# Kernel tuning notes

Hardware: AMD Instinct MI355X
Metric: run time of the kernel (lower is better)

The kernel has to match this reference:

```python
import jax, jax.numpy as jnp
import numpy as np
from math import factorial as _f

LMAX = 2
META = [128, 128, 128]  # input channels per l


def _cg_complex(l1, l2, l3):
    """Condon-Shortley complex Clebsch-Gordan coefficients <l3 m3 | l1 m1 l2 m2>."""
    C = np.zeros((2 * l1 + 1, 2 * l2 + 1, 2 * l3 + 1))
    for m1 in range(-l1, l1 + 1):
        for m2 in range(-l2, l2 + 1):
            m3 = m1 + m2
            if abs(m3) > l3:
                continue
            pre = ((2 * l3 + 1) * _f(l1 + l2 - l3) * _f(l1 - l2 + l3) * _f(-l1 + l2 + l3) / _f(l1 + l2 + l3 + 1)) ** 0.5
            pre *= (_f(l3 + m3) * _f(l3 - m3) * _f(l1 - m1) * _f(l1 + m1) * _f(l2 - m2) * _f(l2 + m2)) ** 0.5
            s = 0.0
            for k in range(0, l1 + l2 - l3 + 1):
                den = [k, l1 + l2 - l3 - k, l1 - m1 - k, l2 + m2 - k, l3 - l2 + m1 + k, l3 - l1 - m2 + k]
                if min(den) < 0:
                    continue
                d = 1.0
                for t in den:
                    d *= _f(t)
                s += (-1) ** k / d
            C[m1 + l1, m2 + l2, m3 + l3] = pre * s
    return C


def _u(l):
    """Complex -> real spherical harmonic change of basis, rows = real m index."""
    U = np.zeros((2 * l + 1, 2 * l + 1), dtype=np.complex128)
    U[l, l] = 1.0
    for m in range(1, l + 1):
        U[l + m, l + m] = (-1) ** m / np.sqrt(2.0)
        U[l + m, l - m] = 1.0 / np.sqrt(2.0)
        U[l - m, l - m] = 1j / np.sqrt(2.0)
        U[l - m, l + m] = -1j * (-1) ** m / np.sqrt(2.0)
    return U


def _cg_real(l1, l2, l3):
    C = _cg_complex(l1, l2, l3).astype(np.complex128)
    R = np.einsum('ai,bj,ck,ijk->abc', _u(l1), _u(l2), np.conj(_u(l3)), C)
    # real-basis CG is purely real or purely imaginary depending on parity of l1+l2+l3
    R = R.imag if np.abs(R.imag).max() > np.abs(R.real).max() else R.real
    return R.astype(np.float32)


# valid couplings (lout-major order, matching the cat layout consumed by repids_tp_out)
LOUT_MAX = 2 * LMAX
COUPLINGS = []
for _lo in range(LOUT_MAX + 1):
    for _l1 in range(LMAX + 1):
        for _l2 in range(LMAX + 1):
            if abs(_l1 - _l2) <= _lo <= _l1 + _l2 and META[_l1] > 0 and META[_l2] > 0:
                COUPLINGS.append((_lo, _l1, _l2, min(META[_l1], META[_l2])))
MIX_OFFS = np.cumsum([0] + [c[3] for c in COUPLINGS])[:-1]
NUM_MIX = int(sum(c[3] for c in COUPLINGS))  # 2432
META_OUT = [max([d for (lo, _, _, d) in COUPLINGS if lo == l], default=0) for l in range(LOUT_MAX + 1)]
CGT = {(l1, l2, lo): _cg_real(l1, l2, lo) for (lo, l1, l2, _) in COUPLINGS}
DIM_IN = int(sum((2 * l + 1) * META[l] for l in range(LMAX + 1)))   # 1152
DIM_OUT = int(sum((2 * l + 1) * META_OUT[l] for l in range(LOUT_MAX + 1)))  # 3200
SQ3 = 3.0 ** 0.5


def setup_inputs() -> dict:
    key = jax.random.key(0)
    k1, k2, k3 = jax.random.split(key, 3)
    B = 16384
    x = jax.random.normal(k1, (B, DIM_IN), dtype=jnp.float32)
    keep_coeff = jax.random.uniform(k2, (sum(META),), dtype=jnp.float32, minval=-SQ3, maxval=SQ3)
    mix_coeff = jax.random.uniform(k3, (NUM_MIX,), dtype=jnp.float32, minval=-SQ3, maxval=SQ3)
    return {"x": x, "keep_coeff": keep_coeff, "mix_coeff": mix_coeff}


def reference(x, keep_coeff, mix_coeff):
    B = x.shape[0]
    # split input rep into per-l blocks, layout is m-major / channel-minor: (B, 2l+1, n_l)
    xs, keep_xs = [], []
    off, coff = 0, 0
    for l in range(LMAX + 1):
        n = META[l]
        sz = (2 * l + 1) * n
        xl = x[:, off:off + sz].reshape(B, 2 * l + 1, n)
        xs.append(xl)
        keep_xs.append(xl * keep_coeff[coff:coff + n])  # k_l \odot x^(l)
        off += sz
        coff += n
    out_blocks = [jnp.zeros((B, 2 * l + 1, META_OUT[l]), x.dtype) for l in range(LOUT_MAX + 1)]
    # CG tensor-product path: 0.5 * s \odot (x ⊗ x), overlapping couplings to same lout are summed
    for (lout, l1, l2, deg), moff in zip(COUPLINGS, MIX_OFFS):
        cg = jnp.asarray(CGT[(l1, l2, lout)])  # (2l1+1, 2l2+1, 2lout+1)
        tp = jnp.einsum('bic,bjc,ijk->bkc', xs[l1][:, :, :deg], xs[l2][:, :, :deg], cg)
        tp = tp * (0.5 * mix_coeff[int(moff):int(moff) + deg])
        out_blocks[lout] = out_blocks[lout].at[:, :, :deg].add(tp)
    # keep (skip) path: copy scaled input channels into the output layout
    for l in range(LMAX + 1):
        ncp = min(META[l], META_OUT[l])
        out_blocks[l] = out_blocks[l].at[:, :, :ncp].add(keep_xs[l][:, :, :ncp])
    return jnp.concatenate([b.reshape(B, -1) for b in out_blocks], axis=1)
```

## Files before the change

### kernel.cpp

```cpp
#include <hip/hip_runtime.h>

namespace cgx {

struct Cplx { double re, im; };

constexpr Cplx cmul(Cplx a, Cplx b) {
  return Cplx{a.re * b.re - a.im * b.im, a.re * b.im + a.im * b.re};
}

constexpr double cfact(int n) {
  double r = 1.0;
  for (int i = 2; i <= n; i++) r *= (double)i;
  return r;
}

constexpr double cabs_(double x) { return x < 0.0 ? -x : x; }

constexpr double csqrt_(double x) {
  if (x <= 0.0) return 0.0;
  double g = x > 1.0 ? x : 1.0;
  for (int it = 0; it < 80; ++it) g = 0.5 * (g + x / g);
  return g;
}

struct CGC { double v[5][5][9]; };

constexpr CGC cg_complex(int l1, int l2, int l3) {
  CGC C{};
  for (int m1 = -l1; m1 <= l1; m1++) {
    for (int m2 = -l2; m2 <= l2; m2++) {
      int m3 = m1 + m2;
      if (m3 < -l3 || m3 > l3) continue;
      double pre = csqrt_((double)(2 * l3 + 1) * cfact(l1 + l2 - l3) *
                          cfact(l1 - l2 + l3) * cfact(-l1 + l2 + l3) /
                          cfact(l1 + l2 + l3 + 1));
      pre *= csqrt_(cfact(l3 + m3) * cfact(l3 - m3) * cfact(l1 - m1) *
                    cfact(l1 + m1) * cfact(l2 - m2) * cfact(l2 + m2));
      double s = 0.0;
      for (int k = 0; k <= l1 + l2 - l3; k++) {
        int d1 = l1 + l2 - l3 - k, d2 = l1 - m1 - k, d3 = l2 + m2 - k;
        int d4 = l3 - l2 + m1 + k, d5 = l3 - l1 - m2 + k;
        if (d1 < 0 || d2 < 0 || d3 < 0 || d4 < 0 || d5 < 0) continue;
        double d = cfact(k) * cfact(d1) * cfact(d2) * cfact(d3) * cfact(d4) * cfact(d5);
        s += ((k & 1) ? -1.0 : 1.0) / d;
      }
      C.v[m1 + l1][m2 + l2][m3 + l3] = pre * s;
    }
  }
  return C;
}

struct UMat { Cplx v[9][9]; };

constexpr UMat umat(int l) {
  UMat U{};
  double is2 = csqrt_(0.5);
  U.v[l][l] = Cplx{1.0, 0.0};
  for (int m = 1; m <= l; m++) {
    double sgn = (m & 1) ? -1.0 : 1.0;
    U.v[l + m][l + m] = Cplx{sgn * is2, 0.0};
    U.v[l + m][l - m] = Cplx{is2, 0.0};
    U.v[l - m][l - m] = Cplx{0.0, is2};
    U.v[l - m][l + m] = Cplx{0.0, -sgn * is2};
  }
  return U;
}

struct CGR { float v[5][5][9]; };

constexpr CGR cg_real(int l1, int l2, int l3) {
  CGC C = cg_complex(l1, l2, l3);
  UMat U1 = umat(l1), U2 = umat(l2), U3 = umat(l3);
  double re[5][5][9]{}, im[5][5][9]{};
  double maxre = 0.0, maxim = 0.0;
  for (int a = 0; a < 2 * l1 + 1; a++)
    for (int b = 0; b < 2 * l2 + 1; b++)
      for (int c = 0; c < 2 * l3 + 1; c++) {
        double ar = 0.0, ai = 0.0;
        for (int i = 0; i < 2 * l1 + 1; i++) {
          Cplx u1 = U1.v[a][i];
          if (u1.re == 0.0 && u1.im == 0.0) continue;
          for (int j = 0; j < 2 * l2 + 1; j++) {
            Cplx u2 = U2.v[b][j];
            if (u2.re == 0.0 && u2.im == 0.0) continue;
            int k0 = (i - l1) + (j - l2) + l3;
            if (k0 < 0 || k0 > 2 * l3) continue;
            double cv = C.v[i][j][k0];
            if (cv == 0.0) continue;
            Cplx u3 = U3.v[c][k0];
            if (u3.re == 0.0 && u3.im == 0.0) continue;
            Cplx u12 = cmul(u1, u2);
            Cplx t = cmul(u12, Cplx{u3.re, -u3.im});
            ar += t.re * cv;
            ai += t.im * cv;
          }
        }
        re[a][b][c] = ar;
        im[a][b][c] = ai;
        if (cabs_(ar) > maxre) maxre = cabs_(ar);
        if (cabs_(ai) > maxim) maxim = cabs_(ai);
      }
  CGR R{};
  bool useim = maxim > maxre;
  for (int a = 0; a < 2 * l1 + 1; a++)
    for (int b = 0; b < 2 * l2 + 1; b++)
      for (int c = 0; c < 2 * l3 + 1; c++)
        R.v[a][b][c] = (float)(useim ? im[a][b][c] : re[a][b][c]);
  return R;
}

}

template <int L1, int L2, int LO>
__device__ __forceinline__ void do_coupling(const float* xa, const float* xb,
                                            float halfmix, float* out) {
  constexpr cgx::CGR t = cgx::cg_real(L1, L2, LO);
#pragma unroll
  for (int k = 0; k < 2 * LO + 1; k++) {
    float tp = 0.0f;
#pragma unroll
    for (int i = 0; i < 2 * L1 + 1; i++) {
#pragma unroll
      for (int j = 0; j < 2 * L2 + 1; j++) {
        const float cv = t.v[i][j][k];
        if (cv > 1e-7f || cv < -1e-7f)
          tp = fmaf(cv * xa[i], xb[j], tp);
      }
    }
    out[k] = fmaf(halfmix, tp, out[k]);
  }
}


__global__ __launch_bounds__(256) void selfmix_kernel(
    const float* __restrict__ x, const float* __restrict__ keep,
    const float* __restrict__ mix, float* __restrict__ out, int B) {
  int tid = blockIdx.x * 256 + threadIdx.x;
  int b = tid >> 7;
  int c = tid & 127;
  if (b >= B) return;

  const float* xb = x + (size_t)b * 1152;
  float x0a[1];
  float x1[3], x2[5];
  x0a[0] = xb[c];
#pragma unroll
  for (int m = 0; m < 3; m++) x1[m] = xb[128 + m * 128 + c];
#pragma unroll
  for (int m = 0; m < 5; m++) x2[m] = xb[512 + m * 128 + c];

  float mx[19];
#pragma unroll
  for (int i = 0; i < 19; i++) mx[i] = 0.5f * mix[i * 128 + c];

  float o0[1], o1[3], o2[5], o3[7], o4[9];
  o0[0] = keep[c] * x0a[0];
  float k1 = keep[128 + c];
#pragma unroll
  for (int m = 0; m < 3; m++) o1[m] = k1 * x1[m];
  float k2 = keep[256 + c];
#pragma unroll
  for (int m = 0; m < 5; m++) o2[m] = k2 * x2[m];
#pragma unroll
  for (int m = 0; m < 7; m++) o3[m] = 0.0f;
#pragma unroll
  for (int m = 0; m < 9; m++) o4[m] = 0.0f;

  do_coupling<0, 0, 0>(x0a, x0a, mx[0], o0);
  do_coupling<1, 1, 0>(x1, x1, mx[1], o0);
  do_coupling<2, 2, 0>(x2, x2, mx[2], o0);

  do_coupling<0, 1, 1>(x0a, x1, mx[3], o1);
  do_coupling<1, 0, 1>(x1, x0a, mx[4], o1);
  do_coupling<1, 1, 1>(x1, x1, mx[5], o1);
  do_coupling<1, 2, 1>(x1, x2, mx[6], o1);
  do_coupling<2, 1, 1>(x2, x1, mx[7], o1);
  do_coupling<2, 2, 1>(x2, x2, mx[8], o1);

  do_coupling<0, 2, 2>(x0a, x2, mx[9], o2);
  do_coupling<1, 1, 2>(x1, x1, mx[10], o2);
  do_coupling<1, 2, 2>(x1, x2, mx[11], o2);
  do_coupling<2, 0, 2>(x2, x0a, mx[12], o2);
  do_coupling<2, 1, 2>(x2, x1, mx[13], o2);
  do_coupling<2, 2, 2>(x2, x2, mx[14], o2);

  do_coupling<1, 2, 3>(x1, x2, mx[15], o3);
  do_coupling<2, 1, 3>(x2, x1, mx[16], o3);
  do_coupling<2, 2, 3>(x2, x2, mx[17], o3);

  do_coupling<2, 2, 4>(x2, x2, mx[18], o4);

  float* ob = out + (size_t)b * 3200;
  ob[c] = o0[0];
#pragma unroll
  for (int m = 0; m < 3; m++) ob[128 + m * 128 + c] = o1[m];
#pragma unroll
  for (int m = 0; m < 5; m++) ob[512 + m * 128 + c] = o2[m];
#pragma unroll
  for (int m = 0; m < 7; m++) ob[1152 + m * 128 + c] = o3[m];
#pragma unroll
  for (int m = 0; m < 9; m++) ob[2048 + m * 128 + c] = o4[m];
}

extern "C" void kernel_launch(void* const* d_in, const int* in_sizes, int n_in,
                              void* d_out, int out_size, void* d_ws, size_t ws_size,
                              hipStream_t stream) {
  const float* x = (const float*)d_in[0];
  const float* keep = (const float*)d_in[1];
  const float* mix = (const float*)d_in[2];
  float* out = (float*)d_out;
  int B = in_sizes[0] / 1152;
  int total = B * 128;
  int blocks = (total + 255) / 256;
  selfmix_kernel<<<blocks, 256, 0, stream>>>(x, keep, mix, out, B);
}
```

Before: 261.8 us.

## Vectorize selfmix kernel to float4 per thread with nontemporal loads and stores

Each thread now processes four adjacent channels using float4 vector types. This cuts the thread count by four and turns global loads and stores into 128-bit accesses. Input and output use nontemporal load/store builtins, and the output blocks are computed and written one group at a time to limit live registers. The cost is more registers per thread and fewer threads in flight to hide memory latency; there is also a small risk that fma contraction now differs from the explicit fmaf used before.

```diff
diff --git a/kernel.cpp b/kernel.cpp
--- a/kernel.cpp
+++ b/kernel.cpp
@@ -111,23 +111,30 @@
 
 }
 
+typedef float v4 __attribute__((ext_vector_type(4)));
+
+__device__ __forceinline__ v4 v4zero() {
+  v4 z = {0.0f, 0.0f, 0.0f, 0.0f};
+  return z;
+}
+
 template <int L1, int L2, int LO>
-__device__ __forceinline__ void do_coupling(const float* xa, const float* xb,
-                                            float halfmix, float* out) {
+__device__ __forceinline__ void do_coupling(const v4* xa, const v4* xb,
+                                            v4 halfmix, v4* out) {
   constexpr cgx::CGR t = cgx::cg_real(L1, L2, LO);
 #pragma unroll
   for (int k = 0; k < 2 * LO + 1; k++) {
-    float tp = 0.0f;
+    v4 tp = v4zero();
 #pragma unroll
     for (int i = 0; i < 2 * L1 + 1; i++) {
 #pragma unroll
       for (int j = 0; j < 2 * L2 + 1; j++) {
         const float cv = t.v[i][j][k];
         if (cv > 1e-7f || cv < -1e-7f)
-          tp = fmaf(cv * xa[i], xb[j], tp);
+          tp = tp + (cv * xa[i]) * xb[j];
       }
     }
-    out[k] = fmaf(halfmix, tp, out[k]);
+    out[k] = out[k] + halfmix * tp;
   }
 }
 
@@ -136,70 +143,87 @@
     const float* __restrict__ x, const float* __restrict__ keep,
     const float* __restrict__ mix, float* __restrict__ out, int B) {
   int tid = blockIdx.x * 256 + threadIdx.x;
-  int b = tid >> 7;
-  int c = tid & 127;
+  int b = tid >> 5;
+  int c0 = (tid & 31) * 4;
   if (b >= B) return;
 
-  const float* xb = x + (size_t)b * 1152;
-  float x0a[1];
-  float x1[3], x2[5];
-  x0a[0] = xb[c];
-#pragma unroll
-  for (int m = 0; m < 3; m++) x1[m] = xb[128 + m * 128 + c];
-#pragma unroll
-  for (int m = 0; m < 5; m++) x2[m] = xb[512 + m * 128 + c];
-
-  float mx[19];
-#pragma unroll
-  for (int i = 0; i < 19; i++) mx[i] = 0.5f * mix[i * 128 + c];
-
-  float o0[1], o1[3], o2[5], o3[7], o4[9];
-  o0[0] = keep[c] * x0a[0];
-  float k1 = keep[128 + c];
-#pragma unroll
-  for (int m = 0; m < 3; m++) o1[m] = k1 * x1[m];
-  float k2 = keep[256 + c];
-#pragma unroll
-  for (int m = 0; m < 5; m++) o2[m] = k2 * x2[m];
-#pragma unroll
-  for (int m = 0; m < 7; m++) o3[m] = 0.0f;
-#pragma unroll
-  for (int m = 0; m < 9; m++) o4[m] = 0.0f;
-
-  do_coupling<0, 0, 0>(x0a, x0a, mx[0], o0);
-  do_coupling<1, 1, 0>(x1, x1, mx[1], o0);
-  do_coupling<2, 2, 0>(x2, x2, mx[2], o0);
-
-  do_coupling<0, 1, 1>(x0a, x1, mx[3], o1);
-  do_coupling<1, 0, 1>(x1, x0a, mx[4], o1);
-  do_coupling<1, 1, 1>(x1, x1, mx[5], o1);
-  do_coupling<1, 2, 1>(x1, x2, mx[6], o1);
-  do_coupling<2, 1, 1>(x2, x1, mx[7], o1);
-  do_coupling<2, 2, 1>(x2, x2, mx[8], o1);
-
-  do_coupling<0, 2, 2>(x0a, x2, mx[9], o2);
-  do_coupling<1, 1, 2>(x1, x1, mx[10], o2);
-  do_coupling<1, 2, 2>(x1, x2, mx[11], o2);
-  do_coupling<2, 0, 2>(x2, x0a, mx[12], o2);
-  do_coupling<2, 1, 2>(x2, x1, mx[13], o2);
-  do_coupling<2, 2, 2>(x2, x2, mx[14], o2);
-
-  do_coupling<1, 2, 3>(x1, x2, mx[15], o3);
-  do_coupling<2, 1, 3>(x2, x1, mx[16], o3);
-  do_coupling<2, 2, 3>(x2, x2, mx[17], o3);
-
-  do_coupling<2, 2, 4>(x2, x2, mx[18], o4);
-
-  float* ob = out + (size_t)b * 3200;
-  ob[c] = o0[0];
-#pragma unroll
-  for (int m = 0; m < 3; m++) ob[128 + m * 128 + c] = o1[m];
-#pragma unroll
-  for (int m = 0; m < 5; m++) ob[512 + m * 128 + c] = o2[m];
-#pragma unroll
-  for (int m = 0; m < 7; m++) ob[1152 + m * 128 + c] = o3[m];
-#pragma unroll
-  for (int m = 0; m < 9; m++) ob[2048 + m * 128 + c] = o4[m];
+  const v4* xr = reinterpret_cast<const v4*>(x + (size_t)b * 1152 + c0);
+  v4* ob = reinterpret_cast<v4*>(out + (size_t)b * 3200 + c0);
+  const v4* kp = reinterpret_cast<const v4*>(keep + c0);
+  const v4* mp = reinterpret_cast<const v4*>(mix + c0);
+  const float half = 0.5f;
+
+  v4 x2[5];
+#pragma unroll
+  for (int m = 0; m < 5; m++) x2[m] = __builtin_nontemporal_load(xr + 128 + m * 32);
+  v4 x1[3];
+#pragma unroll
+  for (int m = 0; m < 3; m++) x1[m] = __builtin_nontemporal_load(xr + 32 + m * 32);
+  v4 x0[1];
+  x0[0] = __builtin_nontemporal_load(xr);
+
+  {
+    v4 o4[9];
+#pragma unroll
+    for (int m = 0; m < 9; m++) o4[m] = v4zero();
+    do_coupling<2, 2, 4>(x2, x2, half * mp[18 * 32], o4);
+#pragma unroll
+    for (int m = 0; m < 9; m++)
+      __builtin_nontemporal_store(o4[m], ob + 512 + m * 32);
+  }
+
+  {
+    v4 o3[7];
+#pragma unroll
+    for (int m = 0; m < 7; m++) o3[m] = v4zero();
+    do_coupling<1, 2, 3>(x1, x2, half * mp[15 * 32], o3);
+    do_coupling<2, 1, 3>(x2, x1, half * mp[16 * 32], o3);
+    do_coupling<2, 2, 3>(x2, x2, half * mp[17 * 32], o3);
+#pragma unroll
+    for (int m = 0; m < 7; m++)
+      __builtin_nontemporal_store(o3[m], ob + 288 + m * 32);
+  }
+
+  {
+    v4 o2[5];
+    v4 k2 = kp[2 * 32];
+#pragma unroll
+    for (int m = 0; m < 5; m++) o2[m] = k2 * x2[m];
+    do_coupling<0, 2, 2>(x0, x2, half * mp[9 * 32], o2);
+    do_coupling<1, 1, 2>(x1, x1, half * mp[10 * 32], o2);
+    do_coupling<1, 2, 2>(x1, x2, half * mp[11 * 32], o2);
+    do_coupling<2, 0, 2>(x2, x0, half * mp[12 * 32], o2);
+    do_coupling<2, 1, 2>(x2, x1, half * mp[13 * 32], o2);
+    do_coupling<2, 2, 2>(x2, x2, half * mp[14 * 32], o2);
+#pragma unroll
+    for (int m = 0; m < 5; m++)
+      __builtin_nontemporal_store(o2[m], ob + 128 + m * 32);
+  }
+
+  {
+    v4 o1[3];
+    v4 k1 = kp[1 * 32];
+#pragma unroll
+    for (int m = 0; m < 3; m++) o1[m] = k1 * x1[m];
+    do_coupling<0, 1, 1>(x0, x1, half * mp[3 * 32], o1);
+    do_coupling<1, 0, 1>(x1, x0, half * mp[4 * 32], o1);
+    do_coupling<1, 1, 1>(x1, x1, half * mp[5 * 32], o1);
+    do_coupling<1, 2, 1>(x1, x2, half * mp[6 * 32], o1);
+    do_coupling<2, 1, 1>(x2, x1, half * mp[7 * 32], o1);
+    do_coupling<2, 2, 1>(x2, x2, half * mp[8 * 32], o1);
+#pragma unroll
+    for (int m = 0; m < 3; m++)
+      __builtin_nontemporal_store(o1[m], ob + 32 + m * 32);
+  }
+
+  {
+    v4 o0[1];
+    o0[0] = kp[0] * x0[0];
+    do_coupling<0, 0, 0>(x0, x0, half * mp[0], o0);
+    do_coupling<1, 1, 0>(x1, x1, half * mp[1 * 32], o0);
+    do_coupling<2, 2, 0>(x2, x2, half * mp[2 * 32], o0);
+    __builtin_nontemporal_store(o0[0], ob);
+  }
 }
 
 extern "C" void kernel_launch(void* const* d_in, const int* in_sizes, int n_in,
@@ -210,7 +234,7 @@
   const float* mix = (const float*)d_in[2];
   float* out = (float*)d_out;
   int B = in_sizes[0] / 1152;
-  int total = B * 128;
+  int total = B * 32;
   int blocks = (total + 255) / 256;
   selfmix_kernel<<<blocks, 256, 0, stream>>>(x, keep, mix, out, B);
 }
```

Measured after the change: 265.0 us. About the same (+1.2%).
